# Optimization experiments

Hardware: AMD Instinct MI355X
Metric: run time of the kernel (lower is better)

Reference implementation:

```python
import jax, jax.numpy as jnp
import numpy as np

B, C, NB, H, W = 4, 128, 4, 256, 256
BT = C // NB  # bottleneck channels = 32
BN1_EPS, BN2_EPS = 1e-5, 1e-3


def setup_inputs() -> dict:
    key = jax.random.key(0)
    ks = jax.random.split(key, 16)
    x = jax.random.normal(ks[0], (B, C, H, W), dtype=jnp.float32)
    w1 = jax.random.normal(ks[1], (BT, C), dtype=jnp.float32) * 0.1
    bn1_gamma = 1.0 + 0.1 * jax.random.normal(ks[2], (BT,), dtype=jnp.float32)
    bn1_beta = 0.1 * jax.random.normal(ks[3], (BT,), dtype=jnp.float32)
    bn1_mean = 0.1 * jax.random.normal(ks[4], (BT,), dtype=jnp.float32)
    bn1_var = 0.5 + jax.random.uniform(ks[5], (BT,), dtype=jnp.float32)
    # learned box extents (vertical x, horizontal y), guaranteed x_max > x_min
    x_min = jax.random.uniform(ks[6], (BT, NB), minval=-100.0, maxval=-2.0)
    x_max = x_min + jax.random.uniform(ks[7], (BT, NB), minval=2.0, maxval=100.0)
    y_min = jax.random.uniform(ks[8], (BT, NB), minval=-100.0, maxval=-2.0)
    y_max = y_min + jax.random.uniform(ks[9], (BT, NB), minval=2.0, maxval=100.0)
    bn2_gamma = 1.0 + 0.1 * jax.random.normal(ks[10], (C,), dtype=jnp.float32)
    bn2_beta = 0.1 * jax.random.normal(ks[11], (C,), dtype=jnp.float32)
    bn2_mean = 0.1 * jax.random.normal(ks[12], (C,), dtype=jnp.float32)
    bn2_var = 0.5 + jax.random.uniform(ks[13], (C,), dtype=jnp.float32)
    return dict(x=x, w1=w1, bn1_gamma=bn1_gamma, bn1_beta=bn1_beta,
                bn1_mean=bn1_mean, bn1_var=bn1_var,
                x_min=x_min, x_max=x_max, y_min=y_min, y_max=y_max,
                bn2_gamma=bn2_gamma, bn2_beta=bn2_beta,
                bn2_mean=bn2_mean, bn2_var=bn2_var)


def _bn(z, gamma, beta, mean, var, eps):
    inv = gamma / jnp.sqrt(var + eps)
    return z * inv[None, :, None, None] + (beta - mean * inv)[None, :, None, None]


def _box_conv(z, x_min, x_max, y_min, y_max):
    """Continuous box-average filter via bilinear sampling of the integral image.
    z: (B, BT, H, W); box params: (BT, NB). Output: (B, BT*NB, H, W)."""
    # zero-padded 2D integral image S[b,c,i,j] = sum z[b,c,:i,:j]  -> (B,BT,H+1,W+1)
    S = jnp.pad(jnp.cumsum(jnp.cumsum(z, axis=2), axis=3),
                ((0, 0), (0, 0), (1, 0), (1, 0)))

    def sample(Sc, u, v):
        # Sc: (B,H+1,W+1); u: (H,), v: (W,) continuous coords into the integral image
        u = jnp.clip(u, 0.0, float(H))
        v = jnp.clip(v, 0.0, float(W))
        i0 = jnp.clip(jnp.floor(u), 0.0, float(H - 1)).astype(jnp.int32)
        j0 = jnp.clip(jnp.floor(v), 0.0, float(W - 1)).astype(jnp.int32)
        wu = u - i0  # fractional weights (carry gradients w.r.t. box params)
        wv = v - j0
        R = Sc[:, i0, :] * (1.0 - wu)[None, :, None] + Sc[:, i0 + 1, :] * wu[None, :, None]
        return R[:, :, j0] * (1.0 - wv)[None, None, :] + R[:, :, j0 + 1] * wv[None, None, :]

    def one_box(Sc, xmn, xmx, ymn, ymx):
        i = jnp.arange(H, dtype=z.dtype)
        j = jnp.arange(W, dtype=z.dtype)
        F11 = sample(Sc, i + xmx, j + ymx)
        F10 = sample(Sc, i + xmx, j + ymn)
        F01 = sample(Sc, i + xmn, j + ymx)
        F00 = sample(Sc, i + xmn, j + ymn)
        area = (xmx - xmn) * (ymx - ymn)
        return (F11 - F10 - F01 + F00) / area  # (B,H,W)

    per_box = jax.vmap(one_box, in_axes=(None, 0, 0, 0, 0))     # over NB
    per_chan = jax.vmap(per_box, in_axes=(1, 0, 0, 0, 0))       # over BT channels
    out = per_chan(S, x_min, x_max, y_min, y_max)               # (BT,NB,B,H,W)
    return out.transpose(2, 0, 1, 3, 4).reshape(z.shape[0], BT * NB, H, W)


def reference(x, w1, bn1_gamma, bn1_beta, bn1_mean, bn1_var,
              x_min, x_max, y_min, y_max,
              bn2_gamma, bn2_beta, bn2_mean, bn2_var):
    # 1x1 conv (no bias)
    h = jnp.einsum('bchw,kc->bkhw', x, w1)
    h = _bn(h, bn1_gamma, bn1_beta, bn1_mean, bn1_var, BN1_EPS)
    h = _box_conv(h, x_min, x_max, y_min, y_max)
    h = _bn(h, bn2_gamma, bn2_beta, bn2_mean, bn2_var, BN2_EPS)
    h = jax.nn.relu(h)
    return jax.nn.relu(x + h)
```

## Files before the change

### kernel.cpp

```cpp
#include <hip/hip_runtime.h>
#include <math.h>

#define BB 4
#define CC 128
#define BT 32
#define NBOX 4
#define HH 256
#define WW 256
#define HW (HH*WW)
#define SP 257
#define SPLANE (SP*SP)
#define NPLANE (BB*BT)
#define CHUNK 32
#define NCHUNK (HH/CHUNK)

__global__ __launch_bounds__(256) void conv_bn1(
        const float* __restrict__ x, const float* __restrict__ w1,
        const float* __restrict__ g1, const float* __restrict__ b1,
        const float* __restrict__ m1, const float* __restrict__ v1,
        float* __restrict__ h) {
    int pix = blockIdx.x * 256 + threadIdx.x;
    int b  = pix >> 16;
    int ij = pix & 65535;
    const float* xb = x + b * (CC * HW) + ij;
    float acc[BT];
    #pragma unroll
    for (int k = 0; k < BT; ++k) acc[k] = 0.f;
    #pragma unroll 4
    for (int c = 0; c < CC; ++c) {
        float xv = xb[c * HW];
        #pragma unroll
        for (int k = 0; k < BT; ++k)
            acc[k] = fmaf(xv, w1[k * CC + c], acc[k]);
    }
    float* hb = h + b * (BT * HW) + ij;
    #pragma unroll
    for (int k = 0; k < BT; ++k) {
        float inv = g1[k] * __frsqrt_rn(v1[k] + 1e-5f);
        float add = b1[k] - m1[k] * inv;
        hb[k * HW] = acc[k] * inv + add;
    }
}

__global__ __launch_bounds__(256) void row_scan(float* __restrict__ t) {
    int wave = threadIdx.x >> 6;
    int lane = threadIdx.x & 63;
    int row = blockIdx.x * 4 + wave;
    float4* rp = (float4*)(t + (size_t)row * WW) + lane;
    float4 v = *rp;
    v.y += v.x; v.z += v.y; v.w += v.z;
    float tot = v.w;
    float sum = tot;
    #pragma unroll
    for (int off = 1; off < 64; off <<= 1) {
        float o = __shfl_up(sum, off, 64);
        if (lane >= off) sum += o;
    }
    float excl = sum - tot;
    v.x += excl; v.y += excl; v.z += excl; v.w += excl;
    *rp = v;
}

__global__ __launch_bounds__(256) void col_partial(const float* __restrict__ t,
                                                   float* __restrict__ T) {
    int plane = blockIdx.x >> 3;
    int chunk = blockIdx.x & 7;
    int j = threadIdx.x;
    const float* tp = t + (size_t)plane * HW + chunk * CHUNK * WW + j;
    float s = 0.f;
    #pragma unroll 8
    for (int r = 0; r < CHUNK; ++r) s += tp[r * WW];
    T[blockIdx.x * 256 + j] = s;
}

__global__ __launch_bounds__(256) void col_final(const float* __restrict__ t,
                                                 const float* __restrict__ T,
                                                 float* __restrict__ s) {
    int plane = blockIdx.x >> 3;
    int chunk = blockIdx.x & 7;
    int j = threadIdx.x;
    float off = 0.f;
    for (int c = 0; c < chunk; ++c) off += T[(plane * 8 + c) * 256 + j];
    const float* tp = t + (size_t)plane * HW + chunk * CHUNK * WW + j;
    float* sp = s + (size_t)plane * SPLANE;
    if (chunk == 0) {
        sp[j + 1] = 0.f;
        if (j == 0) sp[0] = 0.f;
    }
    float run = off;
    int rowbase = chunk * CHUNK;
    #pragma unroll 4
    for (int r = 0; r < CHUNK; ++r) {
        run += tp[r * WW];
        sp[(size_t)(rowbase + r + 1) * SP + j + 1] = run;
        if (j == 0) sp[(size_t)(rowbase + r + 1) * SP] = 0.f;
    }
}

__global__ __launch_bounds__(256) void box_sample(
        const float* __restrict__ s, const float* __restrict__ x,
        const float* __restrict__ xmin, const float* __restrict__ xmax,
        const float* __restrict__ ymin, const float* __restrict__ ymax,
        const float* __restrict__ g2, const float* __restrict__ b2,
        const float* __restrict__ m2, const float* __restrict__ v2,
        float* __restrict__ out) {
    __shared__ float D[SP];
    int bid = blockIdx.x;
    int i = bid & 255;
    int n = (bid >> 8) & 3;
    int k = (bid >> 10) & 31;
    int b = bid >> 15;
    int j = threadIdx.x;
    int kn = k * NBOX + n;
    const float* sp = s + (size_t)(b * BT + k) * SPLANE;

    float xmn = xmin[kn], xmx = xmax[kn], ymn = ymin[kn], ymx = ymax[kn];

    float u_hi = fminf(fmaxf((float)i + xmx, 0.f), 256.f);
    float u_lo = fminf(fmaxf((float)i + xmn, 0.f), 256.f);
    int i1 = (int)fminf(floorf(u_hi), 255.f);
    int i0 = (int)fminf(floorf(u_lo), 255.f);
    float wu1 = u_hi - (float)i1;
    float wu0 = u_lo - (float)i0;

    const float* rA = sp + (size_t)i1 * SP;
    const float* rB = rA + SP;
    const float* rC = sp + (size_t)i0 * SP;
    const float* rD = rC + SP;

    D[j] = rA[j] * (1.f - wu1) + rB[j] * wu1 - rC[j] * (1.f - wu0) - rD[j] * wu0;
    if (j == 0)
        D[256] = rA[256] * (1.f - wu1) + rB[256] * wu1
               - rC[256] * (1.f - wu0) - rD[256] * wu0;
    __syncthreads();

    float v_hi = fminf(fmaxf((float)j + ymx, 0.f), 256.f);
    float v_lo = fminf(fmaxf((float)j + ymn, 0.f), 256.f);
    int j1 = (int)fminf(floorf(v_hi), 255.f);
    int j0 = (int)fminf(floorf(v_lo), 255.f);
    float wv1 = v_hi - (float)j1;
    float wv0 = v_lo - (float)j0;

    float hi = D[j1] * (1.f - wv1) + D[j1 + 1] * wv1;
    float lo = D[j0] * (1.f - wv0) + D[j0 + 1] * wv0;

    float inv = g2[kn] * __frsqrt_rn(v2[kn] + 1e-3f);
    float scale = inv * __frcp_rn((xmx - xmn) * (ymx - ymn));
    float add = b2[kn] - m2[kn] * inv;
    float val = (hi - lo) * scale + add;
    val = fmaxf(val, 0.f);
    size_t oidx = ((size_t)(b * CC + kn) * HH + i) * WW + j;
    out[oidx] = fmaxf(x[oidx] + val, 0.f);
}

extern "C" void kernel_launch(void* const* d_in, const int* in_sizes, int n_in,
                              void* d_out, int out_size, void* d_ws, size_t ws_size,
                              hipStream_t stream) {
    const float* x    = (const float*)d_in[0];
    const float* w1   = (const float*)d_in[1];
    const float* g1   = (const float*)d_in[2];
    const float* b1   = (const float*)d_in[3];
    const float* m1   = (const float*)d_in[4];
    const float* v1   = (const float*)d_in[5];
    const float* xmin = (const float*)d_in[6];
    const float* xmax = (const float*)d_in[7];
    const float* ymin = (const float*)d_in[8];
    const float* ymax = (const float*)d_in[9];
    const float* g2   = (const float*)d_in[10];
    const float* b2   = (const float*)d_in[11];
    const float* m2   = (const float*)d_in[12];
    const float* v2   = (const float*)d_in[13];
    float* out = (float*)d_out;

    float* h = (float*)d_ws;
    float* S = h + (size_t)BB * BT * HW;
    float* T = S + (size_t)NPLANE * SPLANE;

    conv_bn1   <<<(BB * HW) / 256, 256, 0, stream>>>(x, w1, g1, b1, m1, v1, h);
    row_scan   <<<BB * BT * HH / 4, 256, 0, stream>>>(h);
    col_partial<<<NPLANE * NCHUNK, 256, 0, stream>>>(h, T);
    col_final  <<<NPLANE * NCHUNK, 256, 0, stream>>>(h, T, S);
    box_sample <<<BB * BT * NBOX * HH, 256, 0, stream>>>(S, x, xmin, xmax, ymin, ymax,
                                                         g2, b2, m2, v2, out);
}
```

Baseline: 390.5 us.

## Fuse row scan into 1x1 conv and process four rows per box-sample block

The row prefix scan is folded into the 1x1 conv+BN1 kernel. Each block handles one image row, does the scan with wave shuffles and combines the per-wave totals through shared memory, which removes one full read/write pass over the intermediate. The conv weights are staged in LDS instead of being read from global memory per FMA. The box-sample kernel now has each wave handle one output row, so a block covers four rows with four columns per thread, cutting the block count fourfold and amortising per-block setup. The cost is more work and more register pressure per thread in the fused kernel.

```diff
diff --git a/kernel.cpp b/kernel.cpp
--- a/kernel.cpp
+++ b/kernel.cpp
@@ -14,51 +14,57 @@
 #define CHUNK 32
 #define NCHUNK (HH/CHUNK)
 
-__global__ __launch_bounds__(256) void conv_bn1(
+__global__ __launch_bounds__(256) void conv_bn1_rowscan(
         const float* __restrict__ x, const float* __restrict__ w1,
         const float* __restrict__ g1, const float* __restrict__ b1,
         const float* __restrict__ m1, const float* __restrict__ v1,
         float* __restrict__ h) {
-    int pix = blockIdx.x * 256 + threadIdx.x;
-    int b  = pix >> 16;
-    int ij = pix & 65535;
-    const float* xb = x + b * (CC * HW) + ij;
+    __shared__ float w1s[CC * BT];
+    __shared__ float wtot[BT * 4];
+    int b = blockIdx.x >> 8;
+    int i = blockIdx.x & 255;
+    int j = threadIdx.x;
+    int wv = threadIdx.x >> 6;
+    int lane = threadIdx.x & 63;
+
+    #pragma unroll
+    for (int t = 0; t < CC * BT / 256; ++t)
+        w1s[t * 256 + j] = w1[t * 256 + j];
+    __syncthreads();
+
+    const float* xb = x + (size_t)b * (CC * HW) + i * WW + j;
     float acc[BT];
     #pragma unroll
     for (int k = 0; k < BT; ++k) acc[k] = 0.f;
     #pragma unroll 4
     for (int c = 0; c < CC; ++c) {
-        float xv = xb[c * HW];
+        float xv = xb[(size_t)c * HW];
         #pragma unroll
         for (int k = 0; k < BT; ++k)
-            acc[k] = fmaf(xv, w1[k * CC + c], acc[k]);
-    }
-    float* hb = h + b * (BT * HW) + ij;
+            acc[k] = fmaf(xv, w1s[k * CC + c], acc[k]);
+    }
+
     #pragma unroll
     for (int k = 0; k < BT; ++k) {
         float inv = g1[k] * __frsqrt_rn(v1[k] + 1e-5f);
-        float add = b1[k] - m1[k] * inv;
-        hb[k * HW] = acc[k] * inv + add;
-    }
-}
-
-__global__ __launch_bounds__(256) void row_scan(float* __restrict__ t) {
-    int wave = threadIdx.x >> 6;
-    int lane = threadIdx.x & 63;
-    int row = blockIdx.x * 4 + wave;
-    float4* rp = (float4*)(t + (size_t)row * WW) + lane;
-    float4 v = *rp;
-    v.y += v.x; v.z += v.y; v.w += v.z;
-    float tot = v.w;
-    float sum = tot;
-    #pragma unroll
-    for (int off = 1; off < 64; off <<= 1) {
-        float o = __shfl_up(sum, off, 64);
-        if (lane >= off) sum += o;
-    }
-    float excl = sum - tot;
-    v.x += excl; v.y += excl; v.z += excl; v.w += excl;
-    *rp = v;
+        float s = acc[k] * inv + (b1[k] - m1[k] * inv);
+        #pragma unroll
+        for (int off = 1; off < 64; off <<= 1) {
+            float o = __shfl_up(s, off, 64);
+            if (lane >= off) s += o;
+        }
+        acc[k] = s;
+        if (lane == 63) wtot[k * 4 + wv] = s;
+    }
+    __syncthreads();
+
+    float* hb = h + (size_t)b * (BT * HW) + i * WW + j;
+    #pragma unroll
+    for (int k = 0; k < BT; ++k) {
+        float off = 0.f;
+        for (int ww = 0; ww < wv; ++ww) off += wtot[k * 4 + ww];
+        hb[(size_t)k * HW] = acc[k] + off;
+    }
 }
 
 __global__ __launch_bounds__(256) void col_partial(const float* __restrict__ t,
@@ -104,13 +110,14 @@
         const float* __restrict__ g2, const float* __restrict__ b2,
         const float* __restrict__ m2, const float* __restrict__ v2,
         float* __restrict__ out) {
-    __shared__ float D[SP];
+    __shared__ float D[4][SP];
     int bid = blockIdx.x;
-    int i = bid & 255;
-    int n = (bid >> 8) & 3;
-    int k = (bid >> 10) & 31;
-    int b = bid >> 15;
-    int j = threadIdx.x;
+    int wv = threadIdx.x >> 6;
+    int l = threadIdx.x & 63;
+    int i = (bid & 63) * 4 + wv;
+    int n = (bid >> 6) & 3;
+    int k = (bid >> 8) & 31;
+    int b = bid >> 13;
     int kn = k * NBOX + n;
     const float* sp = s + (size_t)(b * BT + k) * SPLANE;
 
@@ -128,29 +135,39 @@
     const float* rC = sp + (size_t)i0 * SP;
     const float* rD = rC + SP;
 
-    D[j] = rA[j] * (1.f - wu1) + rB[j] * wu1 - rC[j] * (1.f - wu0) - rD[j] * wu0;
-    if (j == 0)
-        D[256] = rA[256] * (1.f - wu1) + rB[256] * wu1
-               - rC[256] * (1.f - wu0) - rD[256] * wu0;
+    #pragma unroll
+    for (int c = 0; c < 4; ++c) {
+        int v = l + 64 * c;
+        float a = rA[v], bb = rB[v], cc = rC[v], dd = rD[v];
+        D[wv][v] = (a + wu1 * (bb - a)) - (cc + wu0 * (dd - cc));
+    }
+    if (l == 0) {
+        float a = rA[256], bb = rB[256], cc = rC[256], dd = rD[256];
+        D[wv][256] = (a + wu1 * (bb - a)) - (cc + wu0 * (dd - cc));
+    }
     __syncthreads();
-
-    float v_hi = fminf(fmaxf((float)j + ymx, 0.f), 256.f);
-    float v_lo = fminf(fmaxf((float)j + ymn, 0.f), 256.f);
-    int j1 = (int)fminf(floorf(v_hi), 255.f);
-    int j0 = (int)fminf(floorf(v_lo), 255.f);
-    float wv1 = v_hi - (float)j1;
-    float wv0 = v_lo - (float)j0;
-
-    float hi = D[j1] * (1.f - wv1) + D[j1 + 1] * wv1;
-    float lo = D[j0] * (1.f - wv0) + D[j0 + 1] * wv0;
 
     float inv = g2[kn] * __frsqrt_rn(v2[kn] + 1e-3f);
     float scale = inv * __frcp_rn((xmx - xmn) * (ymx - ymn));
     float add = b2[kn] - m2[kn] * inv;
-    float val = (hi - lo) * scale + add;
-    val = fmaxf(val, 0.f);
-    size_t oidx = ((size_t)(b * CC + kn) * HH + i) * WW + j;
-    out[oidx] = fmaxf(x[oidx] + val, 0.f);
+    size_t obase = ((size_t)(b * CC + kn) * HH + i) * WW;
+
+    #pragma unroll
+    for (int c = 0; c < 4; ++c) {
+        int j = l + 64 * c;
+        float v_hi = fminf(fmaxf((float)j + ymx, 0.f), 256.f);
+        float v_lo = fminf(fmaxf((float)j + ymn, 0.f), 256.f);
+        int j1 = (int)fminf(floorf(v_hi), 255.f);
+        int j0 = (int)fminf(floorf(v_lo), 255.f);
+        float wv1 = v_hi - (float)j1;
+        float wv0 = v_lo - (float)j0;
+        float dh = D[wv][j1], dh1 = D[wv][j1 + 1];
+        float dl = D[wv][j0], dl1 = D[wv][j0 + 1];
+        float hi = dh + wv1 * (dh1 - dh);
+        float lo = dl + wv0 * (dl1 - dl);
+        float val = fmaxf((hi - lo) * scale + add, 0.f);
+        out[obase + j] = fmaxf(x[obase + j] + val, 0.f);
+    }
 }
 
 extern "C" void kernel_launch(void* const* d_in, const int* in_sizes, int n_in,
@@ -176,10 +193,9 @@
     float* S = h + (size_t)BB * BT * HW;
     float* T = S + (size_t)NPLANE * SPLANE;
 
-    conv_bn1   <<<(BB * HW) / 256, 256, 0, stream>>>(x, w1, g1, b1, m1, v1, h);
-    row_scan   <<<BB * BT * HH / 4, 256, 0, stream>>>(h);
+    conv_bn1_rowscan<<<BB * HH, 256, 0, stream>>>(x, w1, g1, b1, m1, v1, h);
     col_partial<<<NPLANE * NCHUNK, 256, 0, stream>>>(h, T);
     col_final  <<<NPLANE * NCHUNK, 256, 0, stream>>>(h, T, S);
-    box_sample <<<BB * BT * NBOX * HH, 256, 0, stream>>>(S, x, xmin, xmax, ymin, ymax,
-                                                         g2, b2, m2, v2, out);
-}
+    box_sample <<<BB * BT * NBOX * HH / 4, 256, 0, stream>>>(S, x, xmin, xmax, ymin, ymax,
+                                                             g2, b2, m2, v2, out);
+}
```

Result: slower. 409.2 us (+4.8%).
